# Performance work log

Hardware: AMD Instinct MI355X
Metric: run time of the kernel (lower is better)

Reference implementation:

```python
import jax, jax.numpy as jnp
import numpy as np

DZ, DB, DS, DX, BATCH, T = 128, 32, 32, 64, 64, 4096


def setup_inputs() -> dict:
    # AW initialized as in PLRNN.init_AW: eye + (1/dz^2) M M^T, spectral norm 1
    rng = np.random.default_rng(0)
    M = rng.standard_normal((DZ, DZ)).astype(np.float32)
    A = np.eye(DZ, dtype=np.float32) + (M @ M.T) / (DZ * DZ)
    A = A / np.max(np.abs(np.linalg.eigvals(A)))
    AW = jnp.asarray(0.95 * A, dtype=jnp.float32)  # 0.95 margin keeps long rollout stable

    key = jax.random.key(0)
    ks = jax.random.split(key, 7)
    z0 = jax.random.normal(ks[0], (BATCH, DZ), dtype=jnp.float32)
    inputs = jax.random.normal(ks[1], (T, DS), dtype=jnp.float32)
    h = 0.1 * jax.random.normal(ks[2], (DZ,), dtype=jnp.float32)
    thetas = 2.0 * jax.random.normal(ks[3], (DZ, DB), dtype=jnp.float32) - 1.0
    alphas = 2.0 * jax.random.normal(ks[4], (DB,), dtype=jnp.float32) - 1.0
    clipping = 5.0 * jnp.ones((DZ, DB), dtype=jnp.float32)  # fixed buffer in torch
    C = 0.1 * jax.random.normal(ks[5], (DZ, DS), dtype=jnp.float32)
    B_obs = jax.random.normal(ks[6], (DZ, DX), dtype=jnp.float32)
    return dict(z0=z0, inputs=inputs, AW=AW, h=h, thetas=thetas,
                alphas=alphas, clipping=clipping, C=C, B_obs=B_obs)


def _leaky(x):
    # nn.LeakyReLU(0.18)
    return jnp.where(x >= 0, x, 0.18 * x)


def reference(z0, inputs, AW, h, thetas, alphas, clipping, C, B_obs):
    # split_diag_offdiag: A = diag(AW), W = AW - diag(AW)
    a_diag = jnp.diag(AW)            # (dz,)
    W = AW - jnp.diag(a_diag)        # (dz, dz), zero diagonal

    def step(z, s):
        # z: (B, dz), s: (ds,)
        d = z[:, :, None] - thetas   # (B, dz, db)
        be = (jnp.sum(alphas * _leaky(d), axis=-1)
              - jnp.sum(alphas * _leaky(d + clipping), axis=-1))  # (B, dz)
        z_new = z * a_diag + be @ W.T + h + (C @ s)  # diag matmul == elementwise
        return z_new, z_new

    _, Z = jax.lax.scan(step, z0, inputs)   # (T, B, dz)
    # torch.cat over list of (B, dz) -> (T*B, dz), time-major
    Z = Z.reshape(-1, Z.shape[-1])
    return Z @ B_obs                        # linear_observation: (T*B, dx)
```

## Files before the change

### kernel.cpp

```cpp
#include <hip/hip_runtime.h>
#include <hip/hip_bf16.h>
#include <hip/hip_fp16.h>

#define DZ 128
#define DB 32
#define DSIN 32
#define DX 64
#define NB 64
#define TT 4096

typedef short v8s __attribute__((ext_vector_type(8)));
typedef float v4f __attribute__((ext_vector_type(4)));
typedef _Float16 v2h __attribute__((ext_vector_type(2)));

__device__ __forceinline__ float pair_sum(float x) {
  int xi = __builtin_bit_cast(int, x);
  int yi = __builtin_amdgcn_mov_dpp(xi, 0xB1, 0xF, 0xF, true);
  return x + __builtin_bit_cast(float, yi);
}

__device__ __forceinline__ short f2bf(float f) {
  __hip_bfloat16 h = __float2bfloat16(f);
  return *reinterpret_cast<short*>(&h);
}

__device__ __forceinline__ v2h pk2h(float a, float b) {
  return __builtin_bit_cast(v2h, __builtin_amdgcn_cvt_pkrtz(a, b));
}
__device__ __forceinline__ float fdot2(v2h a, v2h b, float c) {
  return __builtin_amdgcn_fdot2(a, b, c, false);
}

__global__ void k_prep(const float* __restrict__ AW, const float* __restrict__ alphas,
                       const float* __restrict__ clip, float* __restrict__ WCd) {
  __shared__ float cd[DZ];
  int j = threadIdx.x;
  float s = 0.f;
  for (int k = 0; k < DB; ++k) s = fmaf(alphas[k], clip[j * DB + k], s);
  cd[j] = s;
  __syncthreads();
  float acc = 0.f;
  for (int jj = 0; jj < DZ; ++jj)
    if (jj != j) acc = fmaf(AW[j * DZ + jj], cd[jj], acc);
  WCd[j] = acc;
}

__global__ void k_u(const float* __restrict__ inp, const float* __restrict__ h,
                    const float* __restrict__ C, const float* __restrict__ WCd,
                    float* __restrict__ UT) {
  int gid = blockIdx.x * blockDim.x + threadIdx.x;
  int i = gid >> 10;
  int t0 = (gid & 1023) * 4;
  float base = h[i] - WCd[i];
  const float4* c4 = (const float4*)(C + i * DSIN);
  float4 cv[8];
#pragma unroll
  for (int s = 0; s < 8; ++s) cv[s] = c4[s];
  float out[4];
#pragma unroll
  for (int tt = 0; tt < 4; ++tt) {
    const float4* i4 = (const float4*)(inp + (size_t)(t0 + tt) * DSIN);
    float u = base;
#pragma unroll
    for (int s = 0; s < 8; ++s) {
      float4 iv = i4[s];
      u = fmaf(cv[s].x, iv.x, u);
      u = fmaf(cv[s].y, iv.y, u);
      u = fmaf(cv[s].z, iv.z, u);
      u = fmaf(cv[s].w, iv.w, u);
    }
    out[tt] = u;
  }
  *(float4*)(UT + (size_t)i * TT + t0) = make_float4(out[0], out[1], out[2], out[3]);
}

__global__ __launch_bounds__(256, 1) void k_scan(
    const float* __restrict__ z0, const float* __restrict__ AW,
    const float* __restrict__ thetas, const float* __restrict__ alphas,
    const float* __restrict__ clip, const float* __restrict__ UT,
    short* __restrict__ Z) {
  __shared__ __align__(16) unsigned gpk[2][64];
  const int b = blockIdx.x;
  const int tid = threadIdx.x;
  const int i = tid >> 1, hh = tid & 1;
  const int c0 = hh * 64;

  v2h w[32];
#pragma unroll
  for (int j = 0; j < 32; ++j) {
    float2 a = *(const float2*)(AW + (size_t)i * DZ + c0 + 2 * j);
    float x = (c0 + 2 * j == i) ? 0.f : a.x;
    float y = (c0 + 2 * j + 1 == i) ? 0.f : a.y;
    w[j] = pk2h(x, y);
  }
  const float adiag = AW[(size_t)i * DZ + i];

  v2h th[8], nc[8], al[8];
#pragma unroll
  for (int m = 0; m < 8; ++m) {
    int k = hh * 16 + 2 * m;
    th[m] = pk2h(thetas[i * DB + k], thetas[i * DB + k + 1]);
    nc[m] = pk2h(-clip[i * DB + k], -clip[i * DB + k + 1]);
    al[m] = pk2h(-0.82f * alphas[k], -0.82f * alphas[k + 1]);
  }

  float z = z0[b * DZ + i];
  const float4* up = (const float4*)(UT + (size_t)i * TT);
  float4 ug = up[0];
  short* zp = Z + b * DZ + i;
  const v2h zero2 = pk2h(0.f, 0.f);

#pragma unroll 1
  for (int tg = 0; tg < TT / 4; ++tg) {
    float4 ugn = up[(tg + 1 < TT / 4) ? tg + 1 : tg];
    float uarr[4] = {ug.x, ug.y, ug.z, ug.w};
#pragma unroll
    for (int q = 0; q < 4; ++q) {
      unsigned* gq = gpk[q & 1];
      v2h z2 = pk2h(z, z);
      float g0 = 0.f;
#pragma unroll
      for (int m = 0; m < 8; ++m) {
        v2h d = __builtin_elementwise_min(
            __builtin_elementwise_max(z2 - th[m], nc[m]), zero2);
        g0 = fdot2(al[m], d, g0);
      }
      float gi = pair_sum(g0);
      int pi = __builtin_amdgcn_mov_dpp(__builtin_bit_cast(int, gi), 0xEE, 0xF, 0xF, true);
      unsigned pk = __builtin_bit_cast(unsigned, pk2h(gi, __builtin_bit_cast(float, pi)));
      if ((tid & 3) == 0) gq[tid >> 2] = pk;
      asm volatile("s_waitcnt lgkmcnt(0)\n\ts_barrier" ::: "memory");

      const uint4* g4 = (const uint4*)(gq + hh * 32);
      float m0 = 0.f, m1 = 0.f, m2 = 0.f, m3 = 0.f;
#pragma unroll
      for (int r = 0; r < 8; ++r) {
        uint4 qd = g4[r];
        m0 = fdot2(w[4 * r + 0], __builtin_bit_cast(v2h, qd.x), m0);
        m1 = fdot2(w[4 * r + 1], __builtin_bit_cast(v2h, qd.y), m1);
        m2 = fdot2(w[4 * r + 2], __builtin_bit_cast(v2h, qd.z), m2);
        m3 = fdot2(w[4 * r + 3], __builtin_bit_cast(v2h, qd.w), m3);
      }
      float mm = pair_sum((m0 + m1) + (m2 + m3));
      z = fmaf(z, adiag, mm + uarr[q]);
      if (hh == 0) zp[(size_t)(tg * 4 + q) * (NB * DZ)] = f2bf(z);
    }
    ug = ugn;
  }
}

__global__ __launch_bounds__(256) void k_obs(const short* __restrict__ Z,
                                             const float* __restrict__ Bo,
                                             float* __restrict__ out) {
  const int lane = threadIdx.x & 63;
  const int wv = threadIdx.x >> 6;
  const int rl = lane & 15;
  const int g = lane >> 4;

  v8s bfr[4][4];
#pragma unroll
  for (int nt = 0; nt < 4; ++nt) {
#pragma unroll
    for (int ks = 0; ks < 4; ++ks) {
      v8s f;
#pragma unroll
      for (int m = 0; m < 8; ++m) {
        int k = ks * 32 + g * 8 + m;
        f[m] = f2bf(Bo[k * DX + nt * 16 + rl]);
      }
      bfr[nt][ks] = f;
    }
  }

#pragma unroll
  for (int it = 0; it < 4; ++it) {
    const int r0 = blockIdx.x * 256 + it * 64 + wv * 16;
    const short* zrow = Z + (size_t)(r0 + rl) * DZ;
    v8s afr[4];
#pragma unroll
    for (int ks = 0; ks < 4; ++ks)
      afr[ks] = *(const v8s*)(zrow + ks * 32 + g * 8);
    v4f acc[4];
#pragma unroll
    for (int nt = 0; nt < 4; ++nt) acc[nt] = (v4f){0.f, 0.f, 0.f, 0.f};
#pragma unroll
    for (int nt = 0; nt < 4; ++nt) {
#pragma unroll
      for (int ks = 0; ks < 4; ++ks)
        acc[nt] = __builtin_amdgcn_mfma_f32_16x16x32_bf16(afr[ks], bfr[nt][ks], acc[nt], 0, 0, 0);
    }
#pragma unroll
    for (int nt = 0; nt < 4; ++nt) {
#pragma unroll
      for (int q = 0; q < 4; ++q)
        out[(size_t)(r0 + g * 4 + q) * DX + nt * 16 + rl] = acc[nt][q];
    }
  }
}

extern "C" void kernel_launch(void* const* d_in, const int* in_sizes, int n_in,
                              void* d_out, int out_size, void* d_ws, size_t ws_size,
                              hipStream_t stream) {
  const float* z0 = (const float*)d_in[0];
  const float* inp = (const float*)d_in[1];
  const float* AW = (const float*)d_in[2];
  const float* h = (const float*)d_in[3];
  const float* thetas = (const float*)d_in[4];
  const float* alphas = (const float*)d_in[5];
  const float* clip = (const float*)d_in[6];
  const float* C = (const float*)d_in[7];
  const float* Bo = (const float*)d_in[8];
  float* out = (float*)d_out;

  char* ws = (char*)d_ws;
  float* WCd = (float*)ws;
  float* UT = (float*)(ws + 1024);
  short* Z = (short*)(ws + 1024 + (size_t)TT * DZ * 4);

  k_prep<<<1, 128, 0, stream>>>(AW, alphas, clip, WCd);
  k_u<<<(DZ * TT / 4) / 256, 256, 0, stream>>>(inp, h, C, WCd, UT);
  k_scan<<<NB, 256, 0, stream>>>(z0, AW, thetas, alphas, clip, UT, Z);
  k_obs<<<(TT * NB) / 256, 256, 0, stream>>>(Z, Bo, out);
}
```

Measured before the change: 1.585 ms.

## Split each scan row across four lanes with 512-thread blocks

```diff
diff --git a/kernel.cpp b/kernel.cpp
--- a/kernel.cpp
+++ b/kernel.cpp
@@ -13,10 +13,13 @@
 typedef float v4f __attribute__((ext_vector_type(4)));
 typedef _Float16 v2h __attribute__((ext_vector_type(2)));
 
-__device__ __forceinline__ float pair_sum(float x) {
-  int xi = __builtin_bit_cast(int, x);
-  int yi = __builtin_amdgcn_mov_dpp(xi, 0xB1, 0xF, 0xF, true);
-  return x + __builtin_bit_cast(float, yi);
+__device__ __forceinline__ float dpp_xor1(float x) {
+  int y = __builtin_amdgcn_mov_dpp(__builtin_bit_cast(int, x), 0xB1, 0xF, 0xF, true);
+  return __builtin_bit_cast(float, y);
+}
+__device__ __forceinline__ float dpp_xor2(float x) {
+  int y = __builtin_amdgcn_mov_dpp(__builtin_bit_cast(int, x), 0x4E, 0xF, 0xF, true);
+  return __builtin_bit_cast(float, y);
 }
 
 __device__ __forceinline__ short f2bf(float f) {
@@ -74,20 +77,20 @@
   *(float4*)(UT + (size_t)i * TT + t0) = make_float4(out[0], out[1], out[2], out[3]);
 }
 
-__global__ __launch_bounds__(256, 1) void k_scan(
+__global__ __launch_bounds__(512, 1) void k_scan(
     const float* __restrict__ z0, const float* __restrict__ AW,
     const float* __restrict__ thetas, const float* __restrict__ alphas,
     const float* __restrict__ clip, const float* __restrict__ UT,
     short* __restrict__ Z) {
-  __shared__ __align__(16) unsigned gpk[2][64];
+  __shared__ __align__(16) _Float16 gsh[2][DZ];
   const int b = blockIdx.x;
   const int tid = threadIdx.x;
-  const int i = tid >> 1, hh = tid & 1;
-  const int c0 = hh * 64;
-
-  v2h w[32];
-#pragma unroll
-  for (int j = 0; j < 32; ++j) {
+  const int i = tid >> 2, s = tid & 3;
+  const int c0 = 32 * s;
+
+  v2h w[16];
+#pragma unroll
+  for (int j = 0; j < 16; ++j) {
     float2 a = *(const float2*)(AW + (size_t)i * DZ + c0 + 2 * j);
     float x = (c0 + 2 * j == i) ? 0.f : a.x;
     float y = (c0 + 2 * j + 1 == i) ? 0.f : a.y;
@@ -95,10 +98,10 @@
   }
   const float adiag = AW[(size_t)i * DZ + i];
 
-  v2h th[8], nc[8], al[8];
-#pragma unroll
-  for (int m = 0; m < 8; ++m) {
-    int k = hh * 16 + 2 * m;
+  v2h th[4], nc[4], al[4];
+#pragma unroll
+  for (int m = 0; m < 4; ++m) {
+    int k = 8 * s + 2 * m;
     th[m] = pk2h(thetas[i * DB + k], thetas[i * DB + k + 1]);
     nc[m] = pk2h(-clip[i * DB + k], -clip[i * DB + k + 1]);
     al[m] = pk2h(-0.82f * alphas[k], -0.82f * alphas[k + 1]);
@@ -116,34 +119,40 @@
     float uarr[4] = {ug.x, ug.y, ug.z, ug.w};
 #pragma unroll
     for (int q = 0; q < 4; ++q) {
-      unsigned* gq = gpk[q & 1];
+      _Float16* gq = gsh[q & 1];
       v2h z2 = pk2h(z, z);
-      float g0 = 0.f;
-#pragma unroll
-      for (int m = 0; m < 8; ++m) {
-        v2h d = __builtin_elementwise_min(
+      float g0 = 0.f, g1 = 0.f;
+#pragma unroll
+      for (int m = 0; m < 4; m += 2) {
+        v2h d0 = __builtin_elementwise_min(
             __builtin_elementwise_max(z2 - th[m], nc[m]), zero2);
-        g0 = fdot2(al[m], d, g0);
+        v2h d1 = __builtin_elementwise_min(
+            __builtin_elementwise_max(z2 - th[m + 1], nc[m + 1]), zero2);
+        g0 = fdot2(al[m], d0, g0);
+        g1 = fdot2(al[m + 1], d1, g1);
       }
-      float gi = pair_sum(g0);
-      int pi = __builtin_amdgcn_mov_dpp(__builtin_bit_cast(int, gi), 0xEE, 0xF, 0xF, true);
-      unsigned pk = __builtin_bit_cast(unsigned, pk2h(gi, __builtin_bit_cast(float, pi)));
-      if ((tid & 3) == 0) gq[tid >> 2] = pk;
+      float gf = g0 + g1;
+      gf += dpp_xor1(gf);
+      gf += dpp_xor2(gf);
+      _Float16 ghalf = (_Float16)gf;
+      if (s == 0) gq[i] = ghalf;
       asm volatile("s_waitcnt lgkmcnt(0)\n\ts_barrier" ::: "memory");
 
-      const uint4* g4 = (const uint4*)(gq + hh * 32);
+      const uint4* g4 = ((const uint4*)gq) + 4 * s;
       float m0 = 0.f, m1 = 0.f, m2 = 0.f, m3 = 0.f;
 #pragma unroll
-      for (int r = 0; r < 8; ++r) {
+      for (int r = 0; r < 4; ++r) {
         uint4 qd = g4[r];
         m0 = fdot2(w[4 * r + 0], __builtin_bit_cast(v2h, qd.x), m0);
         m1 = fdot2(w[4 * r + 1], __builtin_bit_cast(v2h, qd.y), m1);
         m2 = fdot2(w[4 * r + 2], __builtin_bit_cast(v2h, qd.z), m2);
         m3 = fdot2(w[4 * r + 3], __builtin_bit_cast(v2h, qd.w), m3);
       }
-      float mm = pair_sum((m0 + m1) + (m2 + m3));
+      float mm = (m0 + m1) + (m2 + m3);
+      mm += dpp_xor1(mm);
+      mm += dpp_xor2(mm);
       z = fmaf(z, adiag, mm + uarr[q]);
-      if (hh == 0) zp[(size_t)(tg * 4 + q) * (NB * DZ)] = f2bf(z);
+      if (s == 0) zp[(size_t)(tg * 4 + q) * (NB * DZ)] = f2bf(z);
     }
     ug = ugn;
   }
@@ -219,6 +228,6 @@
 
   k_prep<<<1, 128, 0, stream>>>(AW, alphas, clip, WCd);
   k_u<<<(DZ * TT / 4) / 256, 256, 0, stream>>>(inp, h, C, WCd, UT);
-  k_scan<<<NB, 256, 0, stream>>>(z0, AW, thetas, alphas, clip, UT, Z);
+  k_scan<<<NB, 512, 0, stream>>>(z0, AW, thetas, alphas, clip, UT, Z);
   k_obs<<<(TT * NB) / 256, 256, 0, stream>>>(Z, Bo, out);
 }
```

Measured after the change: 1.462 ms. 1.08x faster.
